# Kernel optimization log

Measured on AMD Instinct MI355X. Metric: run time of the kernel, lower is better.

The kernel has to match this reference:

```python
import jax, jax.numpy as jnp
import numpy as np

B, F, E, H, D = 8192, 50, 64, 2, 8  # batch, fields, embed, heads, domains
HD = E // H
EPS = 1e-6


def setup_inputs() -> dict:
    key = jax.random.key(0)
    ks = jax.random.split(key, 8)
    std = 0.05  # matches nn.init.normal_(std=0.05) over ALL params (incl. layernorm)
    inputs = jax.random.normal(ks[0], (B, F, E), jnp.float32)
    domain_ids = jax.random.randint(ks[1], (B,), 1, D + 1)  # values 1..D as in torch masks
    W_Query_domains = jax.random.normal(ks[2], (D, E, E), jnp.float32) * std
    W_key = jax.random.normal(ks[3], (E, E), jnp.float32) * std
    W_Value = jax.random.normal(ks[4], (E, E), jnp.float32) * std
    W_Res = jax.random.normal(ks[5], (E, E), jnp.float32) * std
    ln_scale = jax.random.normal(ks[6], (D, E), jnp.float32) * std
    ln_bias = jax.random.normal(ks[7], (D, E), jnp.float32) * std
    return dict(inputs=inputs, domain_ids=domain_ids, W_Query_domains=W_Query_domains,
                W_key=W_key, W_Value=W_Value, W_Res=W_Res,
                ln_scale=ln_scale, ln_bias=ln_bias)


def reference(inputs, domain_ids, W_Query_domains, W_key, W_Value, W_Res, ln_scale, ln_bias):
    # Eval mode: dropouts are identity. merge='no' so shared W_Query is unused.
    b, f, e = inputs.shape
    idx = domain_ids - 1  # 0-based domain index per row

    # Shared keys/values projections
    keys = jnp.einsum('bfe,eo->bfo', inputs, W_key)
    values = jnp.einsum('bfe,eo->bfo', inputs, W_Value)

    # Per-row query weight gather (replaces the python loop over domains)
    Wq = W_Query_domains[idx]  # [B,E,E]
    querys = jnp.einsum('bfe,beo->bfo', inputs, Wq)

    # Split heads: contiguous chunks of size HD along embed dim -> [B,F,H,HD]
    q = querys.reshape(b, f, H, HD)
    k = keys.reshape(b, f, H, HD)
    v = values.reshape(b, f, H, HD)

    scores = jnp.einsum('bihd,bjhd->bhij', q, k) / np.sqrt(HD).astype(np.float32)
    attn = jax.nn.softmax(scores, axis=-1)
    out = jnp.einsum('bhij,bjhd->bihd', attn, v).reshape(b, f, e)  # head concat order matches torch

    out = out + jnp.einsum('bfe,eo->bfo', inputs, W_Res)  # residual via W_Res
    out = jax.nn.relu(out)

    # Per-domain LayerNorm (gather gamma/beta per row)
    gamma = ln_scale[idx][:, None, :]  # [B,1,E]
    beta = ln_bias[idx][:, None, :]
    mean = jnp.mean(out, axis=-1, keepdims=True)
    var = jnp.mean(jnp.square(out - mean), axis=-1, keepdims=True)
    out = (out - mean) * jax.lax.rsqrt(var + EPS) * gamma + beta
    return out
```

## Files before the change

### kernel.cpp

```cpp
#include <hip/hip_runtime.h>
#include <hip/hip_bf16.h>

#define NB    8192
#define NF    50
#define NE    64

typedef __attribute__((ext_vector_type(8))) short short8;
typedef __attribute__((ext_vector_type(4))) short short4v;
typedef __attribute__((ext_vector_type(4))) float float4v;

static constexpr float SM_C   = 0.25509667991878083f;
static constexpr float LN_EPS = 1e-6f;

#define MFMA(a, b, c) __builtin_amdgcn_mfma_f32_16x16x32_bf16((a), (b), (c), 0, 0, 0)

__device__ __forceinline__ unsigned short f2bf(float f) {
    return __bfloat16_as_ushort(__float2bfloat16(f));
}

__device__ __forceinline__ int soff(int row, int col) {
    return row * 64 + ((((col >> 3) ^ row) & 7) << 3) + (col & 7);
}

__device__ __forceinline__ void st_pack4(unsigned short* p, float4v v) {
    union { unsigned short u[4]; short4v s; } r;
    r.u[0] = f2bf(v.x); r.u[1] = f2bf(v.y); r.u[2] = f2bf(v.z); r.u[3] = f2bf(v.w);
    *(short4v*)p = r.s;
}

__device__ __forceinline__ float fexp2(float x) {
#if __has_builtin(__builtin_amdgcn_exp2f)
    return __builtin_amdgcn_exp2f(x);
#else
    float r; asm("v_exp_f32 %0, %1" : "=v"(r) : "v"(x)); return r;
#endif
}

__device__ __forceinline__ float frcp(float x) {
#if __has_builtin(__builtin_amdgcn_rcpf)
    return __builtin_amdgcn_rcpf(x);
#else
    return 1.f / x;
#endif
}

__global__ void prep_weights(const float* __restrict__ wq, const float* __restrict__ wk,
                             const float* __restrict__ wv, const float* __restrict__ wr,
                             unsigned short* __restrict__ ws) {
    int i = blockIdx.x * 256 + threadIdx.x;
    if (i >= 11 * 4096) return;
    int m = i >> 12, t = i & 4095, o = t >> 6, e = t & 63;
    float v;
    if (m < 8) {
        int po = (o & 32) | ((o & 12) << 1) | (((o >> 4) & 1) << 2) | (o & 3);
        v = wq[(m * 64 + e) * 64 + po];
    }
    else if (m == 8) v = wk[e * 64 + o] * SM_C;
    else if (m == 9) v = wv[e * 64 + o];
    else             v = wr[e * 64 + o];
    ws[i] = f2bf(v);
}

__global__ __launch_bounds__(128, 5)
void mdr_mfma(const float* __restrict__ x_g, const int* __restrict__ dom_g,
              const unsigned short* __restrict__ ws,
              const float* __restrict__ gam_g, const float* __restrict__ bet_g,
              float* __restrict__ out_g) {
    __shared__ __align__(16) unsigned short L[2 * NE * NE];

    const int tid = threadIdx.x;
    const int lm  = tid & 15;
    const int lg  = (tid >> 4) & 3;
    const int u   = tid >> 6;
    const int b   = blockIdx.x;

    const int dom = dom_g[b] - 1;
    const float* xb = x_g + (size_t)b * (NF * NE);

    #pragma unroll
    for (int it = 0; it < 8; ++it) {
        int s = tid + it * 128;
        int r = s >> 4, c4 = s & 15;
        float4v v = {0.f, 0.f, 0.f, 0.f};
        if (r < NF) v = *(const float4v*)(xb + s * 4);
        st_pack4(L + soff(r, c4 * 4), v);
    }

    short8 vw[2][2];
    {
        const unsigned short* wv = ws + 9 * 4096;
        #pragma unroll
        for (int i = 0; i < 2; ++i) {
            const int t = u + 2 * i;
            vw[i][0] = *(const short8*)(wv + (lm + 16 * t) * 64 + 8 * lg);
            vw[i][1] = *(const short8*)(wv + (lm + 16 * t) * 64 + 8 * lg + 32);
        }
    }
    __syncthreads();

    short8 xfw[2][2];
    float4v vacc[2][4];
    #pragma unroll
    for (int mt = 0; mt < 4; ++mt) {
        short8 xv0 = *(const short8*)(L + soff(lm + 16 * mt, 8 * lg));
        short8 xv1 = *(const short8*)(L + soff(lm + 16 * mt, 8 * lg + 32));
        if (mt == u)     { xfw[0][0] = xv0; xfw[0][1] = xv1; }
        if (mt == u + 2) { xfw[1][0] = xv0; xfw[1][1] = xv1; }
        #pragma unroll
        for (int i = 0; i < 2; ++i) {
            float4v acc = {0.f, 0.f, 0.f, 0.f};
            acc = MFMA(xv0, vw[i][0], acc);
            vacc[i][mt] = MFMA(xv1, vw[i][1], acc);
        }
    }
    __syncthreads();

    #pragma unroll
    for (int i = 0; i < 2; ++i)
        #pragma unroll
        for (int mt = 0; mt < 4; ++mt)
            st_pack4(L + soff(lm + 16 * (u + 2 * i),
                              32 * (mt >> 1) + 8 * lg + 4 * (mt & 1)),
                     vacc[i][mt]);

    {
        const unsigned short* wk = ws + 8 * 4096;
        #pragma unroll
        for (int mt = 0; mt < 4; ++mt) {
            short8 kw0 = *(const short8*)(wk + (lm + 16 * mt) * 64 + 8 * lg);
            short8 kw1 = *(const short8*)(wk + (lm + 16 * mt) * 64 + 8 * lg + 32);
            #pragma unroll
            for (int i = 0; i < 2; ++i) {
                const int t = u + 2 * i;
                float4v acc = {0.f, 0.f, 0.f, 0.f};
                acc = MFMA(kw0, xfw[i][0], acc);
                acc = MFMA(kw1, xfw[i][1], acc);
                st_pack4(L + 4096 + soff(lm + 16 * t, 16 * mt + 4 * lg), acc);
            }
        }
    }

    short8 qfrag[2][2];
    {
        const unsigned short* wq = ws + dom * 4096;
        #pragma unroll
        for (int i = 0; i < 2; ++i)
            #pragma unroll
            for (int h = 0; h < 2; ++h) {
                float4v a0, a1;
                {
                    short8 q0 = *(const short8*)(wq + (lm + 16 * (2 * h)) * 64 + 8 * lg);
                    short8 q1 = *(const short8*)(wq + (lm + 16 * (2 * h)) * 64 + 8 * lg + 32);
                    float4v z = {0.f, 0.f, 0.f, 0.f};
                    z = MFMA(q0, xfw[i][0], z);
                    a0 = MFMA(q1, xfw[i][1], z);
                }
                {
                    short8 q0 = *(const short8*)(wq + (lm + 16 * (2 * h + 1)) * 64 + 8 * lg);
                    short8 q1 = *(const short8*)(wq + (lm + 16 * (2 * h + 1)) * 64 + 8 * lg + 32);
                    float4v z = {0.f, 0.f, 0.f, 0.f};
                    z = MFMA(q0, xfw[i][0], z);
                    a1 = MFMA(q1, xfw[i][1], z);
                }
                union { unsigned short uu[8]; short8 s; } r;
                #pragma unroll
                for (int r4 = 0; r4 < 4; ++r4) {
                    r.uu[r4]     = f2bf(a0[r4]);
                    r.uu[4 + r4] = f2bf(a1[r4]);
                }
                qfrag[i][h] = r.s;
            }
    }
    __syncthreads();

    float4v oacc[2][4];
    #pragma unroll
    for (int i = 0; i < 2; ++i) {
        short8 pa[2][2];
        #pragma unroll
        for (int h = 0; h < 2; ++h) {
            float p[4][4];
            float sum = 0.f;
            #pragma unroll
            for (int mt = 0; mt < 4; ++mt) {
                short8 kf = *(const short8*)(L + 4096 + soff(lm + 16 * mt, 32 * h + 8 * lg));
                float4v z = {0.f, 0.f, 0.f, 0.f};
                float4v s = MFMA(kf, qfrag[i][h], z);
                #pragma unroll
                for (int r = 0; r < 4; ++r) {
                    float e = fexp2(s[r]);
                    p[mt][r] = e; sum += e;
                }
            }
            sum += __shfl_xor(sum, 16);
            sum += __shfl_xor(sum, 32);
            sum -= 14.f;
            const float ri = frcp(sum);
            #pragma unroll
            for (int ks = 0; ks < 2; ++ks) {
                union { unsigned short uu[8]; short8 s; } r;
                #pragma unroll
                for (int r4 = 0; r4 < 4; ++r4) {
                    r.uu[r4]     = f2bf(p[2 * ks][r4] * ri);
                    r.uu[4 + r4] = f2bf(p[2 * ks + 1][r4] * ri);
                }
                pa[h][ks] = r.s;
            }
        }
        #pragma unroll
        for (int c = 0; c < 4; ++c) {
            oacc[i][c].x = 0.f; oacc[i][c].y = 0.f;
            oacc[i][c].z = 0.f; oacc[i][c].w = 0.f;
        }
        #pragma unroll
        for (int h = 0; h < 2; ++h)
            #pragma unroll
            for (int nt2 = 0; nt2 < 2; ++nt2) {
                const int c = 2 * h + nt2;
                short8 vf0 = *(const short8*)(L + soff(16 * c + lm, 8 * lg));
                short8 vf1 = *(const short8*)(L + soff(16 * c + lm, 8 * lg + 32));
                oacc[i][c] = MFMA(pa[h][0], vf0, oacc[i][c]);
                oacc[i][c] = MFMA(pa[h][1], vf1, oacc[i][c]);
            }
    }

    {
        const unsigned short* wr = ws + 10 * 4096;
        #pragma unroll
        for (int nt = 0; nt < 4; ++nt) {
            short8 rw0 = *(const short8*)(wr + (lm + 16 * nt) * 64 + 8 * lg);
            short8 rw1 = *(const short8*)(wr + (lm + 16 * nt) * 64 + 8 * lg + 32);
            #pragma unroll
            for (int i = 0; i < 2; ++i) {
                oacc[i][nt] = MFMA(xfw[i][0], rw0, oacc[i][nt]);
                oacc[i][nt] = MFMA(xfw[i][1], rw1, oacc[i][nt]);
            }
        }
    }

    float gm[4], bt[4];
    #pragma unroll
    for (int c = 0; c < 4; ++c) {
        gm[c] = gam_g[dom * 64 + 16 * c + lm];
        bt[c] = bet_g[dom * 64 + 16 * c + lm];
    }
    #pragma unroll
    for (int i = 0; i < 2; ++i) {
        const int t = u + 2 * i;
        float v[4][4], s1[4], s2[4];
        #pragma unroll
        for (int r = 0; r < 4; ++r) {
            #pragma unroll
            for (int c = 0; c < 4; ++c) v[r][c] = fmaxf(oacc[i][c][r], 0.f);
            s1[r] = v[r][0] + v[r][1] + v[r][2] + v[r][3];
            s2[r] = v[r][0]*v[r][0] + v[r][1]*v[r][1] + v[r][2]*v[r][2] + v[r][3]*v[r][3];
        }
        #pragma unroll
        for (int msk = 1; msk < 16; msk <<= 1) {
            #pragma unroll
            for (int r = 0; r < 4; ++r) {
                s1[r] += __shfl_xor(s1[r], msk);
                s2[r] += __shfl_xor(s2[r], msk);
            }
        }
        #pragma unroll
        for (int r = 0; r < 4; ++r) {
            const float mean = s1[r] * (1.f / 64.f);
            const float var  = s2[r] * (1.f / 64.f) - mean * mean;
            const float rs   = rsqrtf(var + LN_EPS);
            const int f = 4 * lg + r + 16 * t;
            if (f < NF) {
                float* op = out_g + (size_t)b * (NF * NE) + f * 64 + lm;
                #pragma unroll
                for (int c = 0; c < 4; ++c)
                    op[16 * c] = (v[r][c] - mean) * rs * gm[c] + bt[c];
            }
        }
    }
}

extern "C" void kernel_launch(void* const* d_in, const int* in_sizes, int n_in,
                              void* d_out, int out_size, void* d_ws, size_t ws_size,
                              hipStream_t stream) {
    const float* x   = (const float*)d_in[0];
    const int*   dom = (const int*)  d_in[1];
    const float* wq  = (const float*)d_in[2];
    const float* wk  = (const float*)d_in[3];
    const float* wv  = (const float*)d_in[4];
    const float* wr  = (const float*)d_in[5];
    const float* gam = (const float*)d_in[6];
    const float* bet = (const float*)d_in[7];
    unsigned short* ws = (unsigned short*)d_ws;
    float* out = (float*)d_out;

    hipLaunchKernelGGL(prep_weights, dim3(176), dim3(256), 0, stream, wq, wk, wv, wr, ws);
    hipLaunchKernelGGL(mdr_mfma, dim3(NB), dim3(128), 0, stream,
                       x, dom, ws, gam, bet, out);
}
```

Measured before the change: 93.13 us.

## Keep K fragments in registers and write V to a separate LDS region

Each wave now computes the full key projection for all 64 fields and keeps it in registers as bf16 MFMA fragments, instead of storing keys to LDS and reading them back. To make this work, the key weights are stored column-permuted the same way as the query weights. V is written to the second LDS half right after it is computed, which removes one barrier. The residual and LayerNorm epilogue is fused per row-tile, so only one tile's accumulators are live at a time. In exchange, K projection work is duplicated across the two waves and register pressure rises, so the occupancy hint drops from 5 to 4 blocks.

New measurement: 95.27 us. 1.02x slower.

```diff
diff --git a/kernel.cpp b/kernel.cpp
--- a/kernel.cpp
+++ b/kernel.cpp
@@ -50,18 +50,16 @@
     int i = blockIdx.x * 256 + threadIdx.x;
     if (i >= 11 * 4096) return;
     int m = i >> 12, t = i & 4095, o = t >> 6, e = t & 63;
+    int po = (o & 32) | ((o & 12) << 1) | (((o >> 4) & 1) << 2) | (o & 3);
     float v;
-    if (m < 8) {
-        int po = (o & 32) | ((o & 12) << 1) | (((o >> 4) & 1) << 2) | (o & 3);
-        v = wq[(m * 64 + e) * 64 + po];
-    }
-    else if (m == 8) v = wk[e * 64 + o] * SM_C;
+    if (m < 8)       v = wq[(m * 64 + e) * 64 + po];
+    else if (m == 8) v = wk[e * 64 + po] * SM_C;
     else if (m == 9) v = wv[e * 64 + o];
     else             v = wr[e * 64 + o];
     ws[i] = f2bf(v);
 }
 
-__global__ __launch_bounds__(128, 5)
+__global__ __launch_bounds__(128, 4)
 void mdr_mfma(const float* __restrict__ x_g, const int* __restrict__ dom_g,
               const unsigned short* __restrict__ ws,
               const float* __restrict__ gam_g, const float* __restrict__ bet_g,
@@ -98,44 +96,53 @@
     }
     __syncthreads();
 
-    short8 xfw[2][2];
-    float4v vacc[2][4];
+    short8 xf[4][2];
     #pragma unroll
     for (int mt = 0; mt < 4; ++mt) {
-        short8 xv0 = *(const short8*)(L + soff(lm + 16 * mt, 8 * lg));
-        short8 xv1 = *(const short8*)(L + soff(lm + 16 * mt, 8 * lg + 32));
-        if (mt == u)     { xfw[0][0] = xv0; xfw[0][1] = xv1; }
-        if (mt == u + 2) { xfw[1][0] = xv0; xfw[1][1] = xv1; }
+        xf[mt][0] = *(const short8*)(L + soff(lm + 16 * mt, 8 * lg));
+        xf[mt][1] = *(const short8*)(L + soff(lm + 16 * mt, 8 * lg + 32));
         #pragma unroll
         for (int i = 0; i < 2; ++i) {
             float4v acc = {0.f, 0.f, 0.f, 0.f};
-            acc = MFMA(xv0, vw[i][0], acc);
-            vacc[i][mt] = MFMA(xv1, vw[i][1], acc);
-        }
-    }
-    __syncthreads();
-
-    #pragma unroll
-    for (int i = 0; i < 2; ++i)
-        #pragma unroll
-        for (int mt = 0; mt < 4; ++mt)
-            st_pack4(L + soff(lm + 16 * (u + 2 * i),
-                              32 * (mt >> 1) + 8 * lg + 4 * (mt & 1)),
-                     vacc[i][mt]);
-
+            acc = MFMA(xf[mt][0], vw[i][0], acc);
+            acc = MFMA(xf[mt][1], vw[i][1], acc);
+            st_pack4(L + 4096 + soff(lm + 16 * (u + 2 * i),
+                                     32 * (mt >> 1) + 8 * lg + 4 * (mt & 1)), acc);
+        }
+    }
+
+    short8 xfw[2][2];
+    #pragma unroll
+    for (int k = 0; k < 2; ++k) {
+        xfw[0][k] = u ? xf[1][k] : xf[0][k];
+        xfw[1][k] = u ? xf[3][k] : xf[2][k];
+    }
+
+    short8 kfrag[4][2];
     {
         const unsigned short* wk = ws + 8 * 4096;
+        short8 kwf[4][2];
         #pragma unroll
         for (int mt = 0; mt < 4; ++mt) {
-            short8 kw0 = *(const short8*)(wk + (lm + 16 * mt) * 64 + 8 * lg);
-            short8 kw1 = *(const short8*)(wk + (lm + 16 * mt) * 64 + 8 * lg + 32);
-            #pragma unroll
-            for (int i = 0; i < 2; ++i) {
-                const int t = u + 2 * i;
-                float4v acc = {0.f, 0.f, 0.f, 0.f};
-                acc = MFMA(kw0, xfw[i][0], acc);
-                acc = MFMA(kw1, xfw[i][1], acc);
-                st_pack4(L + 4096 + soff(lm + 16 * t, 16 * mt + 4 * lg), acc);
+            kwf[mt][0] = *(const short8*)(wk + (lm + 16 * mt) * 64 + 8 * lg);
+            kwf[mt][1] = *(const short8*)(wk + (lm + 16 * mt) * 64 + 8 * lg + 32);
+        }
+        #pragma unroll
+        for (int jt = 0; jt < 4; ++jt) {
+            #pragma unroll
+            for (int h = 0; h < 2; ++h) {
+                float4v z0 = {0.f, 0.f, 0.f, 0.f}, z1 = {0.f, 0.f, 0.f, 0.f};
+                z0 = MFMA(kwf[2 * h][0],     xf[jt][0], z0);
+                float4v a0 = MFMA(kwf[2 * h][1],     xf[jt][1], z0);
+                z1 = MFMA(kwf[2 * h + 1][0], xf[jt][0], z1);
+                float4v a1 = MFMA(kwf[2 * h + 1][1], xf[jt][1], z1);
+                union { unsigned short uu[8]; short8 s; } r;
+                #pragma unroll
+                for (int r4 = 0; r4 < 4; ++r4) {
+                    r.uu[r4]     = f2bf(a0[r4]);
+                    r.uu[4 + r4] = f2bf(a1[r4]);
+                }
+                kfrag[jt][h] = r.s;
             }
         }
     }
@@ -173,23 +180,29 @@
     }
     __syncthreads();
 
-    float4v oacc[2][4];
+    float gm[4], bt[4];
+    #pragma unroll
+    for (int c = 0; c < 4; ++c) {
+        gm[c] = gam_g[dom * 64 + 16 * c + lm];
+        bt[c] = bet_g[dom * 64 + 16 * c + lm];
+    }
+
     #pragma unroll
     for (int i = 0; i < 2; ++i) {
+        const int t = u + 2 * i;
         short8 pa[2][2];
         #pragma unroll
         for (int h = 0; h < 2; ++h) {
             float p[4][4];
             float sum = 0.f;
             #pragma unroll
-            for (int mt = 0; mt < 4; ++mt) {
-                short8 kf = *(const short8*)(L + 4096 + soff(lm + 16 * mt, 32 * h + 8 * lg));
+            for (int jt = 0; jt < 4; ++jt) {
                 float4v z = {0.f, 0.f, 0.f, 0.f};
-                float4v s = MFMA(kf, qfrag[i][h], z);
+                float4v s = MFMA(kfrag[jt][h], qfrag[i][h], z);
                 #pragma unroll
                 for (int r = 0; r < 4; ++r) {
                     float e = fexp2(s[r]);
-                    p[mt][r] = e; sum += e;
+                    p[jt][r] = e; sum += e;
                 }
             }
             sum += __shfl_xor(sum, 16);
@@ -207,51 +220,36 @@
                 pa[h][ks] = r.s;
             }
         }
+        float4v oacc[4];
         #pragma unroll
         for (int c = 0; c < 4; ++c) {
-            oacc[i][c].x = 0.f; oacc[i][c].y = 0.f;
-            oacc[i][c].z = 0.f; oacc[i][c].w = 0.f;
+            oacc[c].x = 0.f; oacc[c].y = 0.f; oacc[c].z = 0.f; oacc[c].w = 0.f;
         }
         #pragma unroll
         for (int h = 0; h < 2; ++h)
             #pragma unroll
             for (int nt2 = 0; nt2 < 2; ++nt2) {
                 const int c = 2 * h + nt2;
-                short8 vf0 = *(const short8*)(L + soff(16 * c + lm, 8 * lg));
-                short8 vf1 = *(const short8*)(L + soff(16 * c + lm, 8 * lg + 32));
-                oacc[i][c] = MFMA(pa[h][0], vf0, oacc[i][c]);
-                oacc[i][c] = MFMA(pa[h][1], vf1, oacc[i][c]);
-            }
-    }
-
-    {
-        const unsigned short* wr = ws + 10 * 4096;
-        #pragma unroll
-        for (int nt = 0; nt < 4; ++nt) {
-            short8 rw0 = *(const short8*)(wr + (lm + 16 * nt) * 64 + 8 * lg);
-            short8 rw1 = *(const short8*)(wr + (lm + 16 * nt) * 64 + 8 * lg + 32);
-            #pragma unroll
-            for (int i = 0; i < 2; ++i) {
-                oacc[i][nt] = MFMA(xfw[i][0], rw0, oacc[i][nt]);
-                oacc[i][nt] = MFMA(xfw[i][1], rw1, oacc[i][nt]);
-            }
-        }
-    }
-
-    float gm[4], bt[4];
-    #pragma unroll
-    for (int c = 0; c < 4; ++c) {
-        gm[c] = gam_g[dom * 64 + 16 * c + lm];
-        bt[c] = bet_g[dom * 64 + 16 * c + lm];
-    }
-    #pragma unroll
-    for (int i = 0; i < 2; ++i) {
-        const int t = u + 2 * i;
+                short8 vf0 = *(const short8*)(L + 4096 + soff(16 * c + lm, 8 * lg));
+                short8 vf1 = *(const short8*)(L + 4096 + soff(16 * c + lm, 8 * lg + 32));
+                oacc[c] = MFMA(pa[h][0], vf0, oacc[c]);
+                oacc[c] = MFMA(pa[h][1], vf1, oacc[c]);
+            }
+        {
+            const unsigned short* wr = ws + 10 * 4096;
+            #pragma unroll
+            for (int c = 0; c < 4; ++c) {
+                short8 rw0 = *(const short8*)(wr + (lm + 16 * c) * 64 + 8 * lg);
+                short8 rw1 = *(const short8*)(wr + (lm + 16 * c) * 64 + 8 * lg + 32);
+                oacc[c] = MFMA(xfw[i][0], rw0, oacc[c]);
+                oacc[c] = MFMA(xfw[i][1], rw1, oacc[c]);
+            }
+        }
         float v[4][4], s1[4], s2[4];
         #pragma unroll
         for (int r = 0; r < 4; ++r) {
             #pragma unroll
-            for (int c = 0; c < 4; ++c) v[r][c] = fmaxf(oacc[i][c][r], 0.f);
+            for (int c = 0; c < 4; ++c) v[r][c] = fmaxf(oacc[c][r], 0.f);
             s1[r] = v[r][0] + v[r][1] + v[r][2] + v[r][3];
             s2[r] = v[r][0]*v[r][0] + v[r][1]*v[r][1] + v[r][2]*v[r][2] + v[r][3]*v[r][3];
         }
@@ -268,7 +266,7 @@
             const float mean = s1[r] * (1.f / 64.f);
             const float var  = s2[r] * (1.f / 64.f) - mean * mean;
             const float rs   = rsqrtf(var + LN_EPS);
-            const int f = 4 * lg + r + 16 * t;
+            const int f = 16 * t + 4 * lg + r;
             if (f < NF) {
                 float* op = out_g + (size_t)b * (NF * NE) + f * 64 + lm;
                 #pragma unroll
```
